# Kernel tuning notes

Hardware: AMD Instinct MI355X
Metric: run time of the kernel (lower is better)

The kernel has to match this reference:

```python
import jax, jax.numpy as jnp
import numpy as np

V, E, HID, T = 50000, 300, 256, 9
B, S = 32, 512
H = HID // 2  # per-direction LSTM hidden


def _lstm_dir(x, wih, whh, bih, bhh, reverse):
    # x: [B,S,D]; torch nn.LSTM gate order: i, f, g, o
    bsz = x.shape[0]
    hdim = whh.shape[1]
    xg = jnp.einsum('bsd,gd->bsg', x, wih) + bih + bhh  # [B,S,4H] precomputed input gates

    def step(carry, xt):
        h, c = carry
        g = xt + h @ whh.T
        i, f, gg, o = jnp.split(g, 4, axis=-1)
        c = jax.nn.sigmoid(f) * c + jax.nn.sigmoid(i) * jnp.tanh(gg)
        h = jax.nn.sigmoid(o) * jnp.tanh(c)
        return (h, c), h

    init = (jnp.zeros((bsz, hdim), x.dtype), jnp.zeros((bsz, hdim), x.dtype))
    _, hs = jax.lax.scan(step, init, jnp.swapaxes(xg, 0, 1), reverse=reverse)
    return jnp.swapaxes(hs, 0, 1)  # [B,S,H]


def _crf_nll(emissions, tags, mask, start_t, end_t, trans_t):
    # pytorch-crf: loss = -mean_b llh, llh = numerator - log-partition
    maskf = mask.astype(emissions.dtype)
    em_tag = jnp.take_along_axis(emissions, tags[..., None], axis=2)[..., 0]  # [B,S]
    trans_sc = trans_t[tags[:, :-1], tags[:, 1:]]  # [B,S-1]
    num = start_t[tags[:, 0]] + em_tag[:, 0] + jnp.sum((trans_sc + em_tag[:, 1:]) * maskf[:, 1:], axis=1)
    seq_len = mask.sum(axis=1)
    last_tags = jnp.take_along_axis(tags, (seq_len - 1)[:, None], axis=1)[:, 0]
    num = num + end_t[last_tags]

    def step(alpha, inp):
        em_t, m_t = inp  # [B,T], [B]
        new = jax.nn.logsumexp(alpha[:, :, None] + trans_t[None] + em_t[:, None, :], axis=1)
        return jnp.where(m_t[:, None], new, alpha), None

    alpha0 = start_t[None] + emissions[:, 0]
    alpha, _ = jax.lax.scan(step, alpha0, (jnp.swapaxes(emissions[:, 1:], 0, 1), jnp.swapaxes(mask[:, 1:], 0, 1)))
    denom = jax.nn.logsumexp(alpha + end_t[None], axis=1)
    return -(num - denom).mean()


def _forward(emb, wih0f, whh0f, bih0f, bhh0f, wih0b, whh0b, bih0b, bhh0b,
             wih1f, whh1f, bih1f, bhh1f, wih1b, whh1b, bih1b, bhh1b,
             wproj, bproj, start_t, end_t, trans_t, x, tags, mask):
    e = emb[x]  # [B,S,E]; dropout is identity in eval mode
    h0 = jnp.concatenate([_lstm_dir(e, wih0f, whh0f, bih0f, bhh0f, False),
                          _lstm_dir(e, wih0b, whh0b, bih0b, bhh0b, True)], axis=-1)
    h1 = jnp.concatenate([_lstm_dir(h0, wih1f, whh1f, bih1f, bhh1f, False),
                          _lstm_dir(h0, wih1b, whh1b, bih1b, bhh1b, True)], axis=-1)
    emissions = jnp.einsum('bsh,th->bst', h1, wproj) + bproj  # [B,S,T]
    return _crf_nll(emissions, tags, mask, start_t, end_t, trans_t)


def setup_inputs() -> dict:
    key = jax.random.key(0)
    ks = jax.random.split(key, 32)

    def n(k, shape, s=0.1):
        return jax.random.normal(k, shape, jnp.float32) * s

    d = {}
    d['emb'] = n(ks[0], (V, E)).at[0].set(0.0)  # padding_idx=0 row zeroed
    i = 1
    for l, din in enumerate([E, HID]):
        for dr in 'fb':
            d['wih%d%s' % (l, dr)] = n(ks[i], (4 * H, din)); i += 1
            d['whh%d%s' % (l, dr)] = n(ks[i], (4 * H, H)); i += 1
            d['bih%d%s' % (l, dr)] = n(ks[i], (4 * H,)); i += 1
            d['bhh%d%s' % (l, dr)] = n(ks[i], (4 * H,)); i += 1
    d['wproj'] = n(ks[i], (T, HID)); i += 1
    d['bproj'] = n(ks[i], (T,)); i += 1
    d['start_t'] = n(ks[i], (T,)); i += 1
    d['end_t'] = n(ks[i], (T,)); i += 1
    d['trans_t'] = n(ks[i], (T, T)); i += 1
    d['x'] = jax.random.randint(ks[i], (B, S), 1, V); i += 1
    d['tags'] = jax.random.randint(ks[i], (B, S), 0, T); i += 1
    d['mask'] = jnp.ones((B, S), bool)
    return d


def reference(emb, wih0f, whh0f, bih0f, bhh0f, wih0b, whh0b, bih0b, bhh0b,
              wih1f, whh1f, bih1f, bhh1f, wih1b, whh1b, bih1b, bhh1b,
              wproj, bproj, start_t, end_t, trans_t, x, tags, mask):
    return _forward(emb, wih0f, whh0f, bih0f, bhh0f, wih0b, whh0b, bih0b, bhh0b,
                    wih1f, whh1f, bih1f, bhh1f, wih1b, whh1b, bih1b, bhh1b,
                    wproj, bproj, start_t, end_t, trans_t, x, tags, mask)
```

## Files before the change

### kernel.cpp

```cpp
#include <hip/hip_runtime.h>
#include <hip/hip_bf16.h>

#define Vv 50000
#define Ee 300
#define HIDc 256
#define Tt 9
#define Bb 32
#define Ss 512
#define Hh 128
#define Mtok (Bb*Ss)

__device__ __forceinline__ float sigm(float x) {
    return 1.0f / (1.0f + __expf(-x));
}
__device__ __forceinline__ float tanhx(float x) {
    return 1.0f - 2.0f / (__expf(2.0f * x) + 1.0f);
}

__global__ __launch_bounds__(256) void embed_gather(const float* __restrict__ emb,
                                                    const int* __restrict__ x,
                                                    float* __restrict__ e) {
    int idx = blockIdx.x * 256 + threadIdx.x;
    if (idx >= Mtok * 75) return;
    int token = idx / 75, q = idx % 75;
    ((float4*)e)[idx] = ((const float4*)emb)[(size_t)x[token] * 75 + q];
}

template<int K>
__global__ __launch_bounds__(256) void xg_gemm(const float* __restrict__ A,
                                               const float* __restrict__ Wf, const float* __restrict__ Wb,
                                               const float* __restrict__ bihf, const float* __restrict__ bhhf,
                                               const float* __restrict__ bihb, const float* __restrict__ bhhb,
                                               float* __restrict__ out) {
    constexpr int NKT = (K + 15) / 16;
    const int dir = blockIdx.z;
    const float* W   = dir ? Wb   : Wf;
    const float* bih = dir ? bihb : bihf;
    const float* bhh = dir ? bhhb : bhhf;
    const int m0 = blockIdx.y * 128;
    const int n0 = blockIdx.x * 64;

    __shared__ float As[16][128];
    __shared__ float Bs[16][64];

    const int tid = threadIdx.x;
    const int tx = tid & 15, ty = tid >> 4;
    const int ma = tid & 127, qa = tid >> 7;
    const int nw = tid & 63,  qw = tid >> 6;

    float acc[8][4] = {};

    for (int kt = 0; kt < NKT; ++kt) {
        const int k0 = kt * 16;
        #pragma unroll
        for (int r = 0; r < 2; ++r) {
            int kl = qa * 8 + r * 4;
            float4 v = make_float4(0.f, 0.f, 0.f, 0.f);
            if (k0 + kl < K)
                v = *(const float4*)(A + (size_t)(m0 + ma) * K + k0 + kl);
            As[kl + 0][ma] = v.x; As[kl + 1][ma] = v.y;
            As[kl + 2][ma] = v.z; As[kl + 3][ma] = v.w;
        }
        {
            int kl = qw * 4;
            float4 v = make_float4(0.f, 0.f, 0.f, 0.f);
            if (k0 + kl < K)
                v = *(const float4*)(W + (size_t)(n0 + nw) * K + k0 + kl);
            Bs[kl + 0][nw] = v.x; Bs[kl + 1][nw] = v.y;
            Bs[kl + 2][nw] = v.z; Bs[kl + 3][nw] = v.w;
        }
        __syncthreads();
        #pragma unroll
        for (int k = 0; k < 16; ++k) {
            float4 a0 = *(const float4*)&As[k][ty * 8];
            float4 a1 = *(const float4*)&As[k][ty * 8 + 4];
            float4 b  = *(const float4*)&Bs[k][tx * 4];
            float av[8] = {a0.x, a0.y, a0.z, a0.w, a1.x, a1.y, a1.z, a1.w};
            float bv[4] = {b.x, b.y, b.z, b.w};
            #pragma unroll
            for (int i = 0; i < 8; ++i)
                #pragma unroll
                for (int j = 0; j < 4; ++j)
                    acc[i][j] += av[i] * bv[j];
        }
        __syncthreads();
    }
    #pragma unroll
    for (int j = 0; j < 4; ++j) {
        int n = n0 + tx * 4 + j;
        float bsum = bih[n] + bhh[n];
        #pragma unroll
        for (int i = 0; i < 8; ++i) acc[i][j] += bsum;
    }
    #pragma unroll
    for (int i = 0; i < 8; ++i) {
        int m = m0 + ty * 8 + i;
        *(float4*)(out + ((size_t)dir * Mtok + m) * 512 + n0 + tx * 4) =
            make_float4(acc[i][0], acc[i][1], acc[i][2], acc[i][3]);
    }
}

__global__ __launch_bounds__(512, 1) void lstm_scan(const float* __restrict__ xg,
                                                    const float* __restrict__ whhf,
                                                    const float* __restrict__ whhb,
                                                    float* __restrict__ hout) {
    const int b   = blockIdx.x & 31;
    const int dir = blockIdx.x >> 5;
    const int o   = threadIdx.x;
    const float* whh = dir ? whhb : whhf;

    float w[128];
    const float4* w4 = (const float4*)(whh + (size_t)o * 128);
    #pragma unroll
    for (int q = 0; q < 32; ++q) {
        float4 v = w4[q];
        w[4*q] = v.x; w[4*q+1] = v.y; w[4*q+2] = v.z; w[4*q+3] = v.w;
    }

    __shared__ float h_lds[128];
    __shared__ float g_lds[512];
    float c = 0.f;
    if (o < 128) h_lds[o] = 0.f;
    __syncthreads();

    const float* xgb = xg + ((size_t)dir * Mtok + (size_t)b * Ss) * 512;
    int t = dir ? (Ss - 1) : 0;
    const int dt = dir ? -1 : 1;
    float xv = xgb[(size_t)t * 512 + o];

    for (int step = 0; step < Ss; ++step) {
        float g = xv;
        const float4* h4 = (const float4*)h_lds;
        #pragma unroll
        for (int q = 0; q < 32; ++q) {
            float4 hv = h4[q];
            g += hv.x * w[4*q] + hv.y * w[4*q+1] + hv.z * w[4*q+2] + hv.w * w[4*q+3];
        }
        int tn = t + dt;
        if (step + 1 < Ss) xv = xgb[(size_t)tn * 512 + o];
        g_lds[o] = g;
        __syncthreads();
        if (o < 128) {
            float gi = g_lds[o], gf = g_lds[o + 128], gg = g_lds[o + 256], go = g_lds[o + 384];
            c = sigm(gf) * c + sigm(gi) * tanhx(gg);
            float h = sigm(go) * tanhx(c);
            h_lds[o] = h;
            hout[((size_t)b * Ss + t) * 256 + dir * 128 + o] = h;
        }
        __syncthreads();
        t = tn;
    }
}

__global__ __launch_bounds__(256) void emis_kernel(const float* __restrict__ h1,
                                                   const float* __restrict__ wproj,
                                                   const float* __restrict__ bproj,
                                                   float* __restrict__ em) {
    int idx = blockIdx.x * 256 + threadIdx.x;
    if (idx >= Mtok * Tt) return;
    int token = idx / Tt, tg = idx % Tt;
    const float4* hp = (const float4*)(h1 + (size_t)token * 256);
    const float4* wp = (const float4*)(wproj + (size_t)tg * 256);
    float acc = bproj[tg];
    #pragma unroll 8
    for (int q = 0; q < 64; ++q) {
        float4 a = hp[q], b = wp[q];
        acc += a.x * b.x + a.y * b.y + a.z * b.z + a.w * b.w;
    }
    em[idx] = acc;
}

__global__ __launch_bounds__(256) void crf_num(const float* __restrict__ em,
                                               const int* __restrict__ tags,
                                               const int* __restrict__ mask,
                                               const float* __restrict__ start_t,
                                               const float* __restrict__ end_t,
                                               const float* __restrict__ trans,
                                               float* __restrict__ num) {
    const int b = blockIdx.x;
    const int tid = threadIdx.x;
    __shared__ float sp[256];
    __shared__ int   sc[256];
    float p = 0.f; int cnt = 0;
    for (int t = 1 + tid; t < Ss; t += 256) {
        int mk = mask[b * Ss + t] != 0;
        int tg = tags[b * Ss + t], tp = tags[b * Ss + t - 1];
        if (mk) p += trans[tp * Tt + tg] + em[((size_t)b * Ss + t) * Tt + tg];
        cnt += mk;
    }
    if (tid == 0) cnt += (mask[b * Ss] != 0);
    sp[tid] = p; sc[tid] = cnt;
    __syncthreads();
    for (int s = 128; s > 0; s >>= 1) {
        if (tid < s) { sp[tid] += sp[tid + s]; sc[tid] += sc[tid + s]; }
        __syncthreads();
    }
    if (tid == 0) {
        int t0 = tags[b * Ss];
        float v = start_t[t0] + em[(size_t)b * Ss * Tt + t0] + sp[0];
        int sl = sc[0];
        v += end_t[tags[b * Ss + sl - 1]];
        num[b] = v;
    }
}

__global__ __launch_bounds__(512) void crf_alpha(const float* __restrict__ em,
                                                 const int* __restrict__ mask,
                                                 const float* __restrict__ start_t,
                                                 const float* __restrict__ end_t,
                                                 const float* __restrict__ trans,
                                                 const float* __restrict__ num,
                                                 float* __restrict__ out) {
    __shared__ float al[2][Bb][12];
    __shared__ float tr[Tt * Tt];
    __shared__ float red[Bb];
    const int tid = threadIdx.x;
    if (tid < Tt * Tt) tr[tid] = trans[tid];
    const int b = tid / Tt, j = tid % Tt;
    const bool act = tid < Bb * Tt;
    if (act) al[0][b][j] = start_t[j] + em[(size_t)b * Ss * Tt + j];
    __syncthreads();

    int cur = 0;
    float emn = act ? em[((size_t)b * Ss + 1) * Tt + j] : 0.f;
    for (int t = 1; t < Ss; ++t) {
        float nv = 0.f;
        if (act) {
            float v[Tt];
            float mx = -1e30f;
            #pragma unroll
            for (int i = 0; i < Tt; ++i) {
                v[i] = al[cur][b][i] + tr[i * Tt + j];
                mx = fmaxf(mx, v[i]);
            }
            float s = 0.f;
            #pragma unroll
            for (int i = 0; i < Tt; ++i) s += __expf(v[i] - mx);
            nv = mx + __logf(s) + emn;
            int mk = mask[b * Ss + t] != 0;
            if (t + 1 < Ss) emn = em[((size_t)b * Ss + t + 1) * Tt + j];
            if (!mk) nv = al[cur][b][j];
            al[cur ^ 1][b][j] = nv;
        }
        __syncthreads();
        cur ^= 1;
    }
    if (tid < Bb) {
        float mx = -1e30f;
        float v[Tt];
        #pragma unroll
        for (int jj = 0; jj < Tt; ++jj) {
            v[jj] = al[cur][tid][jj] + end_t[jj];
            mx = fmaxf(mx, v[jj]);
        }
        float s = 0.f;
        #pragma unroll
        for (int jj = 0; jj < Tt; ++jj) s += __expf(v[jj] - mx);
        float denom = mx + __logf(s);
        red[tid] = num[tid] - denom;
    }
    __syncthreads();
    if (tid == 0) {
        float s = 0.f;
        #pragma unroll
        for (int bb = 0; bb < Bb; ++bb) s += red[bb];
        out[0] = -(s / (float)Bb);
    }
}

extern "C" void kernel_launch(void* const* d_in, const int* in_sizes, int n_in,
                              void* d_out, int out_size, void* d_ws, size_t ws_size,
                              hipStream_t stream) {
    const float* emb   = (const float*)d_in[0];
    const float* wih0f = (const float*)d_in[1];  const float* whh0f = (const float*)d_in[2];
    const float* bih0f = (const float*)d_in[3];  const float* bhh0f = (const float*)d_in[4];
    const float* wih0b = (const float*)d_in[5];  const float* whh0b = (const float*)d_in[6];
    const float* bih0b = (const float*)d_in[7];  const float* bhh0b = (const float*)d_in[8];
    const float* wih1f = (const float*)d_in[9];  const float* whh1f = (const float*)d_in[10];
    const float* bih1f = (const float*)d_in[11]; const float* bhh1f = (const float*)d_in[12];
    const float* wih1b = (const float*)d_in[13]; const float* whh1b = (const float*)d_in[14];
    const float* bih1b = (const float*)d_in[15]; const float* bhh1b = (const float*)d_in[16];
    const float* wproj = (const float*)d_in[17]; const float* bproj = (const float*)d_in[18];
    const float* start_t = (const float*)d_in[19];
    const float* end_t   = (const float*)d_in[20];
    const float* trans_t = (const float*)d_in[21];
    const int* x    = (const int*)d_in[22];
    const int* tags = (const int*)d_in[23];
    const int* mask = (const int*)d_in[24];

    float* ws   = (float*)d_ws;
    float* e_buf = ws;
    float* xg    = e_buf + (size_t)Mtok * Ee;
    float* h0    = xg + (size_t)2 * Mtok * 512;
    float* em    = h0 + (size_t)Mtok * 256;
    float* num   = em + (size_t)Mtok * Tt;
    float* h1    = e_buf;
    float* outp  = (float*)d_out;

    embed_gather<<<(Mtok * 75 + 255) / 256, 256, 0, stream>>>(emb, x, e_buf);
    xg_gemm<Ee><<<dim3(8, 128, 2), 256, 0, stream>>>(e_buf, wih0f, wih0b,
                                                     bih0f, bhh0f, bih0b, bhh0b, xg);
    lstm_scan<<<64, 512, 0, stream>>>(xg, whh0f, whh0b, h0);
    xg_gemm<HIDc><<<dim3(8, 128, 2), 256, 0, stream>>>(h0, wih1f, wih1b,
                                                       bih1f, bhh1f, bih1b, bhh1b, xg);
    lstm_scan<<<64, 512, 0, stream>>>(xg, whh1f, whh1b, h1);
    emis_kernel<<<(Mtok * Tt + 255) / 256, 256, 0, stream>>>(h1, wproj, bproj, em);
    crf_num<<<32, 256, 0, stream>>>(em, tags, mask, start_t, end_t, trans_t, num);
    crf_alpha<<<1, 512, 0, stream>>>(em, mask, start_t, end_t, trans_t, num, outp);
}
```

Baseline: 1.793 ms.

## Split LSTM recurrent dot across thread pairs and parallelize gate activations

The recurrent scan now uses 1024 threads per block, with two threads per gate output each computing half of the 128-wide dot product and combining the halves via a shuffle. Each thread keeps only 64 weights in registers, and four independent accumulators shorten the FMA dependency chain. Gate sigmoid/tanh activations are applied by all gate threads in parallel before the sync, leaving only the cell update on the 128 hidden threads. The cost is more LDS traffic per step and a larger block to synchronize.

```diff
diff --git a/kernel.cpp b/kernel.cpp
--- a/kernel.cpp
+++ b/kernel.cpp
@@ -100,52 +100,55 @@
     }
 }
 
-__global__ __launch_bounds__(512, 1) void lstm_scan(const float* __restrict__ xg,
-                                                    const float* __restrict__ whhf,
-                                                    const float* __restrict__ whhb,
-                                                    float* __restrict__ hout) {
+#define W16(F) F(0) F(1) F(2) F(3) F(4) F(5) F(6) F(7) F(8) F(9) F(10) F(11) F(12) F(13) F(14) F(15)
+__global__ __launch_bounds__(1024, 1) void lstm_scan(const float* __restrict__ xg,
+                                                     const float* __restrict__ whhf,
+                                                     const float* __restrict__ whhb,
+                                                     float* __restrict__ hout) {
     const int b   = blockIdx.x & 31;
     const int dir = blockIdx.x >> 5;
-    const int o   = threadIdx.x;
+    const int tid = threadIdx.x;
+    const int o    = tid >> 1;
+    const int half = tid & 1;
     const float* whh = dir ? whhb : whhf;
 
-    float w[128];
-    const float4* w4 = (const float4*)(whh + (size_t)o * 128);
-    #pragma unroll
-    for (int q = 0; q < 32; ++q) {
-        float4 v = w4[q];
-        w[4*q] = v.x; w[4*q+1] = v.y; w[4*q+2] = v.z; w[4*q+3] = v.w;
-    }
+    const float4* wbase = (const float4*)(whh + (size_t)o * 128 + half * 64);
+#define WLOAD(i) const float4 wr##i = wbase[i];
+    W16(WLOAD)
+#undef WLOAD
 
     __shared__ float h_lds[128];
     __shared__ float g_lds[512];
     float c = 0.f;
-    if (o < 128) h_lds[o] = 0.f;
+    if (tid < 128) h_lds[tid] = 0.f;
     __syncthreads();
 
     const float* xgb = xg + ((size_t)dir * Mtok + (size_t)b * Ss) * 512;
     int t = dir ? (Ss - 1) : 0;
     const int dt = dir ? -1 : 1;
     float xv = xgb[(size_t)t * 512 + o];
+    const int cls = o >> 7;
 
     for (int step = 0; step < Ss; ++step) {
-        float g = xv;
-        const float4* h4 = (const float4*)h_lds;
-        #pragma unroll
-        for (int q = 0; q < 32; ++q) {
-            float4 hv = h4[q];
-            g += hv.x * w[4*q] + hv.y * w[4*q+1] + hv.z * w[4*q+2] + hv.w * w[4*q+3];
-        }
+        const float4* h4 = (const float4*)h_lds + half * 16;
+        float g0 = 0.f, g1 = 0.f, g2 = 0.f, g3 = 0.f;
+#define WDOT(i) { float4 hv = h4[i]; g0 += hv.x * wr##i.x; g1 += hv.y * wr##i.y; \
+                  g2 += hv.z * wr##i.z; g3 += hv.w * wr##i.w; }
+        W16(WDOT)
+#undef WDOT
+        float g = (g0 + g1) + (g2 + g3);
+        g += __shfl_xor(g, 1);
+        g += xv;
         int tn = t + dt;
         if (step + 1 < Ss) xv = xgb[(size_t)tn * 512 + o];
-        g_lds[o] = g;
-        __syncthreads();
-        if (o < 128) {
-            float gi = g_lds[o], gf = g_lds[o + 128], gg = g_lds[o + 256], go = g_lds[o + 384];
-            c = sigm(gf) * c + sigm(gi) * tanhx(gg);
-            float h = sigm(go) * tanhx(c);
-            h_lds[o] = h;
-            hout[((size_t)b * Ss + t) * 256 + dir * 128 + o] = h;
+        float act = (cls == 2) ? tanhx(g) : sigm(g);
+        if (half == 0) g_lds[o] = act;
+        __syncthreads();
+        if (tid < 128) {
+            c = g_lds[tid + 128] * c + g_lds[tid] * g_lds[tid + 256];
+            float h = g_lds[tid + 384] * tanhx(c);
+            h_lds[tid] = h;
+            hout[((size_t)b * Ss + t) * 256 + dir * 128 + tid] = h;
         }
         __syncthreads();
         t = tn;
@@ -300,10 +303,10 @@
     embed_gather<<<(Mtok * 75 + 255) / 256, 256, 0, stream>>>(emb, x, e_buf);
     xg_gemm<Ee><<<dim3(8, 128, 2), 256, 0, stream>>>(e_buf, wih0f, wih0b,
                                                      bih0f, bhh0f, bih0b, bhh0b, xg);
-    lstm_scan<<<64, 512, 0, stream>>>(xg, whh0f, whh0b, h0);
+    lstm_scan<<<64, 1024, 0, stream>>>(xg, whh0f, whh0b, h0);
     xg_gemm<HIDc><<<dim3(8, 128, 2), 256, 0, stream>>>(h0, wih1f, wih1b,
                                                        bih1f, bhh1f, bih1b, bhh1b, xg);
-    lstm_scan<<<64, 512, 0, stream>>>(xg, whh1f, whh1b, h1);
+    lstm_scan<<<64, 1024, 0, stream>>>(xg, whh1f, whh1b, h1);
     emis_kernel<<<(Mtok * Tt + 255) / 256, 256, 0, stream>>>(h1, wproj, bproj, em);
     crf_num<<<32, 256, 0, stream>>>(em, tags, mask, start_t, end_t, trans_t, num);
     crf_alpha<<<1, 512, 0, stream>>>(em, mask, start_t, end_t, trans_t, num, outp);
```

Result: slower. 1.973 ms (+10.0%).

## Store LSTM recurrent weights as fp16 in LDS and use fdot2

Applied to the files above, without the earlier changes.

The recurrent scan kernel now converts W_hh to fp16 and keeps it in shared memory in a k-chunked layout instead of 128 fp32 registers per thread. The hidden state is also packed as fp16, and the matvec uses the packed fp16 dot-product instruction with four accumulators. Gate nonlinearities move to all 512 threads before the barrier, so the 128-thread cell update has less serial work. This aims to relieve register pressure and shorten the per-step critical path, at the cost of fp16 rounding of the weights and hidden state across 512 recurrent steps.

```diff
diff --git a/kernel.cpp b/kernel.cpp
--- a/kernel.cpp
+++ b/kernel.cpp
@@ -10,11 +10,31 @@
 #define Hh 128
 #define Mtok (Bb*Ss)
 
+#define LSTM_NODOT2 0
+
 __device__ __forceinline__ float sigm(float x) {
     return 1.0f / (1.0f + __expf(-x));
 }
 __device__ __forceinline__ float tanhx(float x) {
     return 1.0f - 2.0f / (__expf(2.0f * x) + 1.0f);
+}
+
+typedef _Float16 half2v __attribute__((ext_vector_type(2)));
+
+__device__ __forceinline__ unsigned short f2h_bits(float x) {
+    union { _Float16 h; unsigned short s; } u;
+    u.h = (_Float16)x;
+    return u.s;
+}
+
+__device__ __forceinline__ float dot2(unsigned int w, unsigned int h, float acc) {
+    union { unsigned int u; half2v v; } a, b;
+    a.u = w; b.u = h;
+#if LSTM_NODOT2
+    return acc + (float)a.v.x * (float)b.v.x + (float)a.v.y * (float)b.v.y;
+#else
+    return __builtin_amdgcn_fdot2(a.v, b.v, acc, false);
+#endif
 }
 
 __global__ __launch_bounds__(256) void embed_gather(const float* __restrict__ emb,
@@ -106,46 +126,49 @@
                                                     float* __restrict__ hout) {
     const int b   = blockIdx.x & 31;
     const int dir = blockIdx.x >> 5;
-    const int o   = threadIdx.x;
+    const int tid = threadIdx.x;
+    const int o   = tid;
     const float* whh = dir ? whhb : whhf;
 
-    float w[128];
-    const float4* w4 = (const float4*)(whh + (size_t)o * 128);
-    #pragma unroll
-    for (int q = 0; q < 32; ++q) {
-        float4 v = w4[q];
-        w[4*q] = v.x; w[4*q+1] = v.y; w[4*q+2] = v.z; w[4*q+3] = v.w;
-    }
-
-    __shared__ float h_lds[128];
-    __shared__ float g_lds[512];
+    __shared__ unsigned short wlds16[16 * 512 * 8];
+    __shared__ unsigned int   hp[64];
+    __shared__ float          g_lds[512];
+
+    for (int e = tid; e < 512 * 128; e += 512) {
+        int ro = e >> 7, k = e & 127;
+        wlds16[((k >> 3) * 512 + ro) * 8 + (k & 7)] = f2h_bits(whh[e]);
+    }
+    if (tid < 64) hp[tid] = 0u;
     float c = 0.f;
-    if (o < 128) h_lds[o] = 0.f;
     __syncthreads();
 
     const float* xgb = xg + ((size_t)dir * Mtok + (size_t)b * Ss) * 512;
     int t = dir ? (Ss - 1) : 0;
     const int dt = dir ? -1 : 1;
     float xv = xgb[(size_t)t * 512 + o];
+    const int cls = o >> 7;
 
     for (int step = 0; step < Ss; ++step) {
-        float g = xv;
-        const float4* h4 = (const float4*)h_lds;
-        #pragma unroll
-        for (int q = 0; q < 32; ++q) {
-            float4 hv = h4[q];
-            g += hv.x * w[4*q] + hv.y * w[4*q+1] + hv.z * w[4*q+2] + hv.w * w[4*q+3];
-        }
+        float a0 = 0.f, a1 = 0.f, a2 = 0.f, a3 = 0.f;
+        #pragma unroll
+        for (int kc = 0; kc < 16; ++kc) {
+            uint4 wv = *(const uint4*)(wlds16 + ((kc * 512 + o) * 8));
+            uint4 hv = *(const uint4*)((const unsigned short*)hp + kc * 8);
+            a0 = dot2(wv.x, hv.x, a0);
+            a1 = dot2(wv.y, hv.y, a1);
+            a2 = dot2(wv.z, hv.z, a2);
+            a3 = dot2(wv.w, hv.w, a3);
+        }
+        float g = ((a0 + a1) + (a2 + a3)) + xv;
         int tn = t + dt;
         if (step + 1 < Ss) xv = xgb[(size_t)tn * 512 + o];
-        g_lds[o] = g;
-        __syncthreads();
-        if (o < 128) {
-            float gi = g_lds[o], gf = g_lds[o + 128], gg = g_lds[o + 256], go = g_lds[o + 384];
-            c = sigm(gf) * c + sigm(gi) * tanhx(gg);
-            float h = sigm(go) * tanhx(c);
-            h_lds[o] = h;
-            hout[((size_t)b * Ss + t) * 256 + dir * 128 + o] = h;
+        g_lds[o] = (cls == 2) ? tanhx(g) : sigm(g);
+        __syncthreads();
+        if (tid < 128) {
+            c = g_lds[tid + 128] * c + g_lds[tid] * g_lds[tid + 256];
+            float h = g_lds[tid + 384] * tanhx(c);
+            hout[((size_t)b * Ss + t) * 256 + dir * 128 + tid] = h;
+            ((unsigned short*)hp)[tid] = f2h_bits(h);
         }
         __syncthreads();
         t = tn;
```

Measured after the change: 1.468 ms. -18.1%, faster.
